# Performance work log

Hardware: AMD Instinct MI355X
Metric: run time of the kernel (lower is better)

Reference implementation:

```python
import jax, jax.numpy as jnp
import numpy as np

N = 100000  # nodes
E = 1600000  # edges
F_IN, F_HID, F_OUT = 64, 128, 128


def _glorot(key, shape):
    fan_in, fan_out = shape[1], shape[0]
    lim = float(np.sqrt(6.0 / (fan_in + fan_out)))
    return jax.random.uniform(key, shape, jnp.float32, -lim, lim)


def setup_inputs() -> dict:
    key = jax.random.key(0)
    ks = jax.random.split(key, 8)
    x = jax.random.normal(ks[0], (N, F_IN), jnp.float32)
    edge_index = jax.random.randint(ks[1], (2, E), 0, N, jnp.int64)
    # SAGEConv params: lin_l (neighbors, with bias), lin_r (root, no bias)
    return {
        "x": x,
        "edge_index": edge_index,
        "W1_l": _glorot(ks[2], (F_HID, F_IN)),
        "b1": jnp.zeros((F_HID,), jnp.float32),
        "W1_r": _glorot(ks[3], (F_HID, F_IN)),
        "W2_l": _glorot(ks[4], (F_OUT, F_HID)),
        "b2": jnp.zeros((F_OUT,), jnp.float32),
        "W2_r": _glorot(ks[5], (F_OUT, F_HID)),
    }


def _sage_conv(x, src, dst, deg_inv, W_l, b, W_r):
    # mean aggregation of source features onto target nodes
    agg = jax.ops.segment_sum(x[src], dst, num_segments=N)  # [N, F]
    agg = agg * deg_inv[:, None]
    return agg @ W_l.T + b + x @ W_r.T


def reference(x, edge_index, W1_l, b1, W1_r, W2_l, b2, W2_r):
    src, dst = edge_index[0], edge_index[1]
    deg = jax.ops.segment_sum(jnp.ones((E,), jnp.float32), dst, num_segments=N)
    deg_inv = 1.0 / jnp.maximum(deg, 1.0)
    h = _sage_conv(x, src, dst, deg_inv, W1_l, b1, W1_r)
    h = jax.nn.relu(h)
    # dropout p=0.5 is identity in eval mode
    out = _sage_conv(h, src, dst, deg_inv, W2_l, b2, W2_r)
    return out
```

## Files before the change

kernel.cpp:

```cpp
#include <hip/hip_runtime.h>
#include <hip/hip_bf16.h>

__device__ __forceinline__ float b2f(unsigned short u) {
  return __uint_as_float(((unsigned int)u) << 16);
}
__device__ __forceinline__ unsigned short f2b(float f) {
  unsigned int x = __float_as_uint(f);
  unsigned int r = x + 0x7FFFu + ((x >> 16) & 1u);
  return (unsigned short)(r >> 16);
}
__device__ __forceinline__ unsigned int pack2(float lo, float hi) {
  return (unsigned int)f2b(lo) | ((unsigned int)f2b(hi) << 16);
}

typedef short bf16x8 __attribute__((ext_vector_type(8)));
typedef float f32x4 __attribute__((ext_vector_type(4)));

#define CHUNK 8192
#define NBUCKP 1024

__global__ void detect_kernel(const void* __restrict__ x_raw,
                              const void* __restrict__ idx_raw,
                              int* __restrict__ hdr) {
  int lane = threadIdx.x;
  const unsigned short* xb = (const unsigned short*)x_raw;
  unsigned short u = xb[2 * lane];
  int e = (u >> 7) & 0xFF;
  bool sane = ((u & 0x7FFFu) == 0) || (e >= 107 && e <= 137);
  unsigned long long m = __ballot(sane);
  const int* ib = (const int*)idx_raw;
  int v = ib[2 * lane + 1];
  unsigned long long m2 = __ballot(v != 0);
  if (lane == 0) {
    hdr[0] = (__popcll(m) >= 32) ? 0 : 1;
    hdr[1] = (m2 == 0ull) ? 1 : 0;
  }
}

__global__ void convert_w_kernel(const void* __restrict__ W1l, const void* __restrict__ W1r,
                                 const void* __restrict__ W2l, const void* __restrict__ W2r,
                                 const void* __restrict__ b1, const void* __restrict__ b2,
                                 const int* __restrict__ hdr,
                                 unsigned short* __restrict__ W1l_h, unsigned short* __restrict__ W1r_h,
                                 unsigned short* __restrict__ W2l_h, unsigned short* __restrict__ W2r_h,
                                 float* __restrict__ b1_f, float* __restrict__ b2_f) {
  int i = blockIdx.x * blockDim.x + threadIdx.x;
  const void* s; unsigned short* dh = nullptr; float* df = nullptr; int off;
  if (i < 8192)       { s = W1l; dh = W1l_h; off = i; }
  else if (i < 16384) { s = W1r; dh = W1r_h; off = i - 8192; }
  else if (i < 32768) { s = W2l; dh = W2l_h; off = i - 16384; }
  else if (i < 49152) { s = W2r; dh = W2r_h; off = i - 32768; }
  else if (i < 49280) { s = b1;  df = b1_f;  off = i - 49152; }
  else if (i < 49408) { s = b2;  df = b2_f;  off = i - 49280; }
  else return;
  float v = hdr[0] ? ((const float*)s)[off] : b2f(((const unsigned short*)s)[off]);
  if (dh) dh[off] = f2b(v);
  else df[off] = v;
}

__global__ void convert_x_kernel(const void* __restrict__ x_raw,
                                 const int* __restrict__ hdr,
                                 unsigned short* __restrict__ xc, int n_elems) {
  int i = blockIdx.x * blockDim.x + threadIdx.x;
  if (i >= n_elems) return;
  xc[i] = hdr[0] ? f2b(((const float*)x_raw)[i]) : ((const unsigned short*)x_raw)[i];
}

__global__ __launch_bounds__(256) void hist_chunks_kernel(
    const int* __restrict__ idx_raw, const int* __restrict__ hdr,
    int* __restrict__ H, int n_edges, int NC) {
  __shared__ int h[NBUCKP];
  for (int i = threadIdx.x; i < NBUCKP; i += 256) h[i] = 0;
  __syncthreads();
  const int c = blockIdx.x;
  const bool i64 = hdr[1];
  const int base = c * CHUNK;
  #pragma unroll
  for (int t = 0; t < CHUNK / 256; ++t) {
    int e = base + t * 256 + threadIdx.x;
    if (e < n_edges) {
      int d = i64 ? idx_raw[2 * (n_edges + e)] : idx_raw[n_edges + e];
      atomicAdd(&h[d >> 7], 1);
    }
  }
  __syncthreads();
  for (int i = threadIdx.x; i < NBUCKP; i += 256) H[(size_t)i * NC + c] = h[i];
}

__global__ __launch_bounds__(256) void gscan_sums_kernel(const int* __restrict__ arr,
                                                         int* __restrict__ blockSums, int n) {
  __shared__ int ws[4];
  int tid = threadIdx.x, lane = tid & 63, wid = tid >> 6;
  int base = blockIdx.x * 2048 + tid * 8;
  int s = 0;
  #pragma unroll
  for (int t = 0; t < 8; ++t) {
    int i = base + t;
    if (i < n) s += arr[i];
  }
  #pragma unroll
  for (int m = 1; m < 64; m <<= 1) s += __shfl_xor(s, m, 64);
  if (lane == 0) ws[wid] = s;
  __syncthreads();
  if (tid == 0) blockSums[blockIdx.x] = ws[0] + ws[1] + ws[2] + ws[3];
}

__global__ void gscan_offsets_kernel(const int* __restrict__ blockSums,
                                     int* __restrict__ blockOffs, int nb) {
  int lane = threadIdx.x;
  int carry = 0;
  for (int start = 0; start < nb; start += 64) {
    int i = start + lane;
    int v = (i < nb) ? blockSums[i] : 0;
    int isc = v;
    #pragma unroll
    for (int off = 1; off < 64; off <<= 1) {
      int t = __shfl_up(isc, off, 64);
      if (lane >= off) isc += t;
    }
    if (i < nb) blockOffs[i] = carry + isc - v;
    carry += __shfl(isc, 63, 64);
  }
}

__global__ __launch_bounds__(256) void gscan_emit_kernel(const int* __restrict__ arr,
                                                         const int* __restrict__ blockOffs,
                                                         int* __restrict__ out, int n) {
  __shared__ int ws[4];
  int tid = threadIdx.x, lane = tid & 63, wid = tid >> 6;
  int base = blockIdx.x * 2048 + tid * 8;
  int v[8];
  int s = 0;
  #pragma unroll
  for (int t = 0; t < 8; ++t) {
    int i = base + t;
    v[t] = (i < n) ? arr[i] : 0;
    s += v[t];
  }
  int isc = s;
  #pragma unroll
  for (int off = 1; off < 64; off <<= 1) {
    int t = __shfl_up(isc, off, 64);
    if (lane >= off) isc += t;
  }
  if (lane == 63) ws[wid] = isc;
  __syncthreads();
  int wb = 0;
  #pragma unroll
  for (int w = 0; w < 4; ++w)
    if (w < wid) wb += ws[w];
  int excl = blockOffs[blockIdx.x] + wb + isc - s;
  #pragma unroll
  for (int t = 0; t < 8; ++t) {
    int i = base + t;
    if (i < n) {
      out[i] = excl;
      excl += v[t];
    }
  }
}

__global__ __launch_bounds__(256) void scatter_kernel(
    const int* __restrict__ idx_raw, const int* __restrict__ hdr,
    const int* __restrict__ O, unsigned long long* __restrict__ ebuf,
    int n_edges, int NC) {
  __shared__ int base[NBUCKP];
  const int c = blockIdx.x;
  for (int i = threadIdx.x; i < NBUCKP; i += 256) base[i] = O[(size_t)i * NC + c];
  __syncthreads();
  const bool i64 = hdr[1];
  const int eb = c * CHUNK;
  #pragma unroll
  for (int t = 0; t < CHUNK / 256; ++t) {
    int e = eb + t * 256 + threadIdx.x;
    if (e < n_edges) {
      int s = i64 ? idx_raw[2 * e] : idx_raw[e];
      int d = i64 ? idx_raw[2 * (n_edges + e)] : idx_raw[n_edges + e];
      int pos = atomicAdd(&base[d >> 7], 1);
      ebuf[pos] = (unsigned long long)(unsigned)s | ((unsigned long long)(unsigned)d << 32);
    }
  }
}

__global__ __launch_bounds__(256) void bucket_csr_kernel(
    const unsigned long long* __restrict__ ebuf, const int* __restrict__ O,
    int* __restrict__ col, int* __restrict__ row_start, float* __restrict__ deg_inv,
    int n_nodes, int n_edges, int NC) {
  __shared__ int cntl[128];
  __shared__ int cur[128];
  __shared__ int w0tot;
  const int b = blockIdx.x, tid = threadIdx.x;
  const int node0 = b << 7;
  const int beg = O[(size_t)b * NC];
  const int end = (b + 1 < NBUCKP) ? O[(size_t)(b + 1) * NC] : n_edges;
  if (tid < 128) cntl[tid] = 0;
  __syncthreads();
  for (int e = beg + tid; e < end; e += 256) {
    int d = (int)(ebuf[e] >> 32);
    atomicAdd(&cntl[d - node0], 1);
  }
  __syncthreads();
  int v = (tid < 128) ? cntl[tid] : 0;
  int lane = tid & 63;
  int isc = v;
  #pragma unroll
  for (int o = 1; o < 64; o <<= 1) {
    int t = __shfl_up(isc, o, 64);
    if (lane >= o) isc += t;
  }
  if (tid == 63) w0tot = isc;
  __syncthreads();
  int incl = isc + ((tid >= 64 && tid < 128) ? w0tot : 0);
  int excl = incl - v;
  if (tid < 128) {
    cur[tid] = excl;
    int node = node0 + tid;
    if (node < n_nodes) {
      row_start[node] = beg + excl;
      deg_inv[node] = 1.0f / (float)((v > 1) ? v : 1);
    }
  }
  __syncthreads();
  for (int e = beg + tid; e < end; e += 256) {
    unsigned long long u = ebuf[e];
    int s = (int)(u & 0xFFFFFFFFull);
    int d = (int)(u >> 32);
    int r = atomicAdd(&cur[d - node0], 1);
    col[beg + r] = s;
  }
  if (b == 0 && tid == 0) row_start[n_nodes] = n_edges;
}

__global__ __launch_bounds__(256) void gather1_kernel(
    const unsigned short* __restrict__ xc, const int* __restrict__ row_start,
    const int* __restrict__ col, const float* __restrict__ deg_inv,
    unsigned short* __restrict__ agg1, int n_nodes) {
  int lane = threadIdx.x & 63;
  int n = blockIdx.x * 4 + (threadIdx.x >> 6);
  if (n >= n_nodes) return;
  int rg = lane >> 3, fq = lane & 7;
  int beg = row_start[n], end = row_start[n + 1];
  float a[8];
  #pragma unroll
  for (int t = 0; t < 8; ++t) a[t] = 0.f;
  int i = beg;
  for (; i + 15 < end; i += 16) {
    int s0 = col[i + rg], s1 = col[i + 8 + rg];
    uint4 p = *(const uint4*)(xc + (size_t)s0 * 64 + fq * 8);
    uint4 q = *(const uint4*)(xc + (size_t)s1 * 64 + fq * 8);
    a[0] += b2f(p.x & 0xFFFF); a[1] += b2f(p.x >> 16);
    a[2] += b2f(p.y & 0xFFFF); a[3] += b2f(p.y >> 16);
    a[4] += b2f(p.z & 0xFFFF); a[5] += b2f(p.z >> 16);
    a[6] += b2f(p.w & 0xFFFF); a[7] += b2f(p.w >> 16);
    a[0] += b2f(q.x & 0xFFFF); a[1] += b2f(q.x >> 16);
    a[2] += b2f(q.y & 0xFFFF); a[3] += b2f(q.y >> 16);
    a[4] += b2f(q.z & 0xFFFF); a[5] += b2f(q.z >> 16);
    a[6] += b2f(q.w & 0xFFFF); a[7] += b2f(q.w >> 16);
  }
  for (; i < end; i += 8) {
    if (i + rg < end) {
      int s0 = col[i + rg];
      uint4 p = *(const uint4*)(xc + (size_t)s0 * 64 + fq * 8);
      a[0] += b2f(p.x & 0xFFFF); a[1] += b2f(p.x >> 16);
      a[2] += b2f(p.y & 0xFFFF); a[3] += b2f(p.y >> 16);
      a[4] += b2f(p.z & 0xFFFF); a[5] += b2f(p.z >> 16);
      a[6] += b2f(p.w & 0xFFFF); a[7] += b2f(p.w >> 16);
    }
  }
  #pragma unroll
  for (int m = 8; m < 64; m <<= 1)
    #pragma unroll
    for (int t = 0; t < 8; ++t) a[t] += __shfl_xor(a[t], m, 64);
  if (rg == 0) {
    float di = deg_inv[n];
    uint4 o;
    o.x = pack2(a[0] * di, a[1] * di);
    o.y = pack2(a[2] * di, a[3] * di);
    o.z = pack2(a[4] * di, a[5] * di);
    o.w = pack2(a[6] * di, a[7] * di);
    *(uint4*)(agg1 + (size_t)n * 64 + fq * 8) = o;
  }
}

__global__ __launch_bounds__(256) void gather2_kernel(
    const unsigned short* __restrict__ h, const int* __restrict__ row_start,
    const int* __restrict__ col, const float* __restrict__ deg_inv,
    unsigned short* __restrict__ agg2, int n_nodes) {
  int lane = threadIdx.x & 63;
  int n = blockIdx.x * 4 + (threadIdx.x >> 6);
  if (n >= n_nodes) return;
  int rg = lane >> 4, fq = lane & 15;
  int beg = row_start[n], end = row_start[n + 1];
  float a[8];
  #pragma unroll
  for (int t = 0; t < 8; ++t) a[t] = 0.f;
  int i = beg;
  for (; i + 7 < end; i += 8) {
    int s0 = col[i + rg], s1 = col[i + 4 + rg];
    uint4 p = *(const uint4*)(h + (size_t)s0 * 128 + fq * 8);
    uint4 q = *(const uint4*)(h + (size_t)s1 * 128 + fq * 8);
    a[0] += b2f(p.x & 0xFFFF); a[1] += b2f(p.x >> 16);
    a[2] += b2f(p.y & 0xFFFF); a[3] += b2f(p.y >> 16);
    a[4] += b2f(p.z & 0xFFFF); a[5] += b2f(p.z >> 16);
    a[6] += b2f(p.w & 0xFFFF); a[7] += b2f(p.w >> 16);
    a[0] += b2f(q.x & 0xFFFF); a[1] += b2f(q.x >> 16);
    a[2] += b2f(q.y & 0xFFFF); a[3] += b2f(q.y >> 16);
    a[4] += b2f(q.z & 0xFFFF); a[5] += b2f(q.z >> 16);
    a[6] += b2f(q.w & 0xFFFF); a[7] += b2f(q.w >> 16);
  }
  for (; i < end; i += 4) {
    if (i + rg < end) {
      int s0 = col[i + rg];
      uint4 p = *(const uint4*)(h + (size_t)s0 * 128 + fq * 8);
      a[0] += b2f(p.x & 0xFFFF); a[1] += b2f(p.x >> 16);
      a[2] += b2f(p.y & 0xFFFF); a[3] += b2f(p.y >> 16);
      a[4] += b2f(p.z & 0xFFFF); a[5] += b2f(p.z >> 16);
      a[6] += b2f(p.w & 0xFFFF); a[7] += b2f(p.w >> 16);
    }
  }
  #pragma unroll
  for (int m = 16; m < 64; m <<= 1)
    #pragma unroll
    for (int t = 0; t < 8; ++t) a[t] += __shfl_xor(a[t], m, 64);
  if (rg == 0) {
    float di = deg_inv[n];
    uint4 o;
    o.x = pack2(a[0] * di, a[1] * di);
    o.y = pack2(a[2] * di, a[3] * di);
    o.z = pack2(a[4] * di, a[5] * di);
    o.w = pack2(a[6] * di, a[7] * di);
    *(uint4*)(agg2 + (size_t)n * 128 + fq * 8) = o;
  }
}

template <int K1, int K2, bool RELU, bool FINAL>
__global__ __launch_bounds__(256, 4) void gemm_mfma(
    const unsigned short* __restrict__ A1, const unsigned short* __restrict__ A2,
    const unsigned short* __restrict__ Wl, const unsigned short* __restrict__ Wr,
    const float* __restrict__ bias,
    unsigned short* __restrict__ Cb, void* __restrict__ Cf,
    const int* __restrict__ hdr, int n_nodes) {
  const int tid = threadIdx.x;
  const int wave = tid >> 6, lane = tid & 63;
  const int m16 = lane & 15, quad = lane >> 4;
  const int nb = blockIdx.x * 128 + wave * 32;
  int row0 = nb + m16;      if (row0 >= n_nodes) row0 = n_nodes - 1;
  int row1 = nb + 16 + m16; if (row1 >= n_nodes) row1 = n_nodes - 1;

  f32x4 acc[2][8];
  #pragma unroll
  for (int mi = 0; mi < 2; ++mi)
    #pragma unroll
    for (int ji = 0; ji < 8; ++ji) acc[mi][ji] = (f32x4){0.f, 0.f, 0.f, 0.f};

  constexpr int NSTEP = (K1 + K2) / 32;
  #pragma unroll
  for (int c = 0; c < NSTEP; ++c) {
    const bool first = (c * 32) < K1;
    const unsigned short* A = first ? A1 : A2;
    const unsigned short* W = first ? Wl : Wr;
    const int kb = first ? c * 32 : c * 32 - K1;
    const int Krow = first ? K1 : K2;
    const int ko = kb + quad * 8;
    bf16x8 a0 = *(const bf16x8*)(A + (size_t)row0 * Krow + ko);
    bf16x8 a1 = *(const bf16x8*)(A + (size_t)row1 * Krow + ko);
    bf16x8 w[8];
    #pragma unroll
    for (int ji = 0; ji < 8; ++ji)
      w[ji] = *(const bf16x8*)(W + (size_t)(ji * 16 + m16) * Krow + ko);
    #pragma unroll
    for (int ji = 0; ji < 8; ++ji) {
      acc[0][ji] = __builtin_amdgcn_mfma_f32_16x16x32_bf16(a0, w[ji], acc[0][ji], 0, 0, 0);
      acc[1][ji] = __builtin_amdgcn_mfma_f32_16x16x32_bf16(a1, w[ji], acc[1][ji], 0, 0, 0);
    }
  }

  const bool f32out = FINAL && (hdr[0] == 1);
  #pragma unroll
  for (int ji = 0; ji < 8; ++ji) {
    int j = ji * 16 + m16;
    float bj = bias[j];
    #pragma unroll
    for (int mi = 0; mi < 2; ++mi) {
      #pragma unroll
      for (int r = 0; r < 4; ++r) {
        int n = nb + mi * 16 + quad * 4 + r;
        if (n >= n_nodes) continue;
        float v = acc[mi][ji][r] + bj;
        if (RELU) v = fmaxf(v, 0.f);
        if (FINAL) {
          if (f32out) ((float*)Cf)[(size_t)n * 128 + j] = v;
          else ((unsigned short*)Cf)[(size_t)n * 128 + j] = f2b(v);
        } else {
          Cb[(size_t)n * 128 + j] = f2b(v);
        }
      }
    }
  }
}

extern "C" void kernel_launch(void* const* d_in, const int* in_sizes, int n_in,
                              void* d_out, int out_size, void* d_ws, size_t ws_size,
                              hipStream_t stream) {
  const void* x_raw  = d_in[0];
  const int* idx_raw = (const int*)d_in[1];
  const void* W1l = d_in[2];
  const void* b1  = d_in[3];
  const void* W1r = d_in[4];
  const void* W2l = d_in[5];
  const void* b2  = d_in[6];
  const void* W2r = d_in[7];
  const int N = in_sizes[0] / 64;
  const int E = in_sizes[1] / 2;
  const int NC = (E + CHUNK - 1) / CHUNK;
  const int NSCAN = NBUCKP * NC;
  const int NBs = (NSCAN + 2047) / 2048;
  const int NBUCK = (N + 127) >> 7;

  char* ws = (char*)d_ws;
  size_t off = 0;
  auto alloc = [&](size_t bytes) {
    char* p = ws + off;
    off = (off + bytes + 511) & ~((size_t)511);
    return p;
  };
  int* hdr        = (int*)alloc(512);
  int* H          = (int*)alloc((size_t)NSCAN * 4);
  int* O          = (int*)alloc((size_t)NSCAN * 4);
  int* blockSums  = (int*)alloc((size_t)NBs * 4);
  int* blockOffs  = (int*)alloc((size_t)NBs * 4);
  unsigned long long* ebuf = (unsigned long long*)alloc((size_t)E * 8);
  int* col        = (int*)alloc((size_t)E * 4);
  int* row_start  = (int*)alloc(((size_t)N + 1) * 4);
  float* deg_inv  = (float*)alloc((size_t)N * 4);
  unsigned short* W1l_h = (unsigned short*)alloc(16384);
  unsigned short* W1r_h = (unsigned short*)alloc(16384);
  unsigned short* W2l_h = (unsigned short*)alloc(32768);
  unsigned short* W2r_h = (unsigned short*)alloc(32768);
  float* b1_f     = (float*)alloc(512);
  float* b2_f     = (float*)alloc(512);
  unsigned short* xc   = (unsigned short*)alloc((size_t)N * 64 * 2);
  unsigned short* agg1 = (unsigned short*)alloc((size_t)N * 64 * 2);
  unsigned short* hbuf = (unsigned short*)alloc((size_t)N * 128 * 2);
  unsigned short* agg2 = (unsigned short*)alloc((size_t)N * 128 * 2);

  detect_kernel<<<1, 64, 0, stream>>>(x_raw, idx_raw, hdr);
  convert_w_kernel<<<(49408 + 255) / 256, 256, 0, stream>>>(
      W1l, W1r, W2l, W2r, b1, b2, hdr, W1l_h, W1r_h, W2l_h, W2r_h, b1_f, b2_f);
  convert_x_kernel<<<(N * 64 + 255) / 256, 256, 0, stream>>>(x_raw, hdr, xc, N * 64);
  hist_chunks_kernel<<<NC, 256, 0, stream>>>(idx_raw, hdr, H, E, NC);
  gscan_sums_kernel<<<NBs, 256, 0, stream>>>(H, blockSums, NSCAN);
  gscan_offsets_kernel<<<1, 64, 0, stream>>>(blockSums, blockOffs, NBs);
  gscan_emit_kernel<<<NBs, 256, 0, stream>>>(H, blockOffs, O, NSCAN);
  scatter_kernel<<<NC, 256, 0, stream>>>(idx_raw, hdr, O, ebuf, E, NC);
  bucket_csr_kernel<<<NBUCK, 256, 0, stream>>>(ebuf, O, col, row_start, deg_inv, N, E, NC);
  gather1_kernel<<<(N + 3) / 4, 256, 0, stream>>>(xc, row_start, col, deg_inv, agg1, N);
  gemm_mfma<64, 64, true, false><<<(N + 127) / 128, 256, 0, stream>>>(
      agg1, xc, W1l_h, W1r_h, b1_f, hbuf, nullptr, hdr, N);
  gather2_kernel<<<(N + 3) / 4, 256, 0, stream>>>(hbuf, row_start, col, deg_inv, agg2, N);
  gemm_mfma<128, 128, false, true><<<(N + 127) / 128, 256, 0, stream>>>(
      agg2, hbuf, W2l_h, W2r_h, b2_f, nullptr, d_out, hdr, N);
}
```

Baseline: 338.5 us.

## Vectorize edge index loads and restructure gather kernels for more loads in flight

The histogram and scatter kernels now read edge indices as uint4 vectors, one per thread, instead of scalar strided loads. gather1 maps two nodes per wavefront, each handled by a half-wave, which shortens the shuffle reduction. Both gather kernels unroll to four outstanding row loads per iteration and use a cheaper bf16-to-float unpack helper. The aim is fewer memory instructions and more memory-level parallelism in the gathers, at the cost of more registers and alignment assumptions on the index buffer.

```diff
diff --git a/kernel.cpp b/kernel.cpp
--- a/kernel.cpp
+++ b/kernel.cpp
@@ -11,6 +11,12 @@
 }
 __device__ __forceinline__ unsigned int pack2(float lo, float hi) {
   return (unsigned int)f2b(lo) | ((unsigned int)f2b(hi) << 16);
+}
+__device__ __forceinline__ void acc8(float* a, uint4 p) {
+  a[0] += __uint_as_float(p.x << 16); a[1] += __uint_as_float(p.x & 0xFFFF0000u);
+  a[2] += __uint_as_float(p.y << 16); a[3] += __uint_as_float(p.y & 0xFFFF0000u);
+  a[4] += __uint_as_float(p.z << 16); a[5] += __uint_as_float(p.z & 0xFFFF0000u);
+  a[6] += __uint_as_float(p.w << 16); a[7] += __uint_as_float(p.w & 0xFFFF0000u);
 }
 
 typedef short bf16x8 __attribute__((ext_vector_type(8)));
@@ -73,14 +79,33 @@
   for (int i = threadIdx.x; i < NBUCKP; i += 256) h[i] = 0;
   __syncthreads();
   const int c = blockIdx.x;
-  const bool i64 = hdr[1];
   const int base = c * CHUNK;
-  #pragma unroll
-  for (int t = 0; t < CHUNK / 256; ++t) {
-    int e = base + t * 256 + threadIdx.x;
-    if (e < n_edges) {
-      int d = i64 ? idx_raw[2 * (n_edges + e)] : idx_raw[n_edges + e];
-      atomicAdd(&h[d >> 7], 1);
+  const int lim = min(n_edges - base, CHUNK);
+  if (hdr[1]) {
+    const uint4* dp = (const uint4*)(idx_raw + 2 * (size_t)n_edges + 2 * (size_t)base);
+    #pragma unroll
+    for (int t = 0; t < CHUNK / 512; ++t) {
+      int q = t * 256 + threadIdx.x;
+      int e = 2 * q;
+      if (e < lim) {
+        uint4 v = dp[q];
+        atomicAdd(&h[((int)v.x) >> 7], 1);
+        if (e + 1 < lim) atomicAdd(&h[((int)v.z) >> 7], 1);
+      }
+    }
+  } else {
+    const uint4* dp = (const uint4*)(idx_raw + (size_t)n_edges + base);
+    #pragma unroll
+    for (int t = 0; t < CHUNK / 1024; ++t) {
+      int q = t * 256 + threadIdx.x;
+      int e = 4 * q;
+      if (e < lim) {
+        uint4 v = dp[q];
+        atomicAdd(&h[((int)v.x) >> 7], 1);
+        if (e + 1 < lim) atomicAdd(&h[((int)v.y) >> 7], 1);
+        if (e + 2 < lim) atomicAdd(&h[((int)v.z) >> 7], 1);
+        if (e + 3 < lim) atomicAdd(&h[((int)v.w) >> 7], 1);
+      }
     }
   }
   __syncthreads();
@@ -168,16 +193,49 @@
   const int c = blockIdx.x;
   for (int i = threadIdx.x; i < NBUCKP; i += 256) base[i] = O[(size_t)i * NC + c];
   __syncthreads();
-  const bool i64 = hdr[1];
   const int eb = c * CHUNK;
-  #pragma unroll
-  for (int t = 0; t < CHUNK / 256; ++t) {
-    int e = eb + t * 256 + threadIdx.x;
-    if (e < n_edges) {
-      int s = i64 ? idx_raw[2 * e] : idx_raw[e];
-      int d = i64 ? idx_raw[2 * (n_edges + e)] : idx_raw[n_edges + e];
-      int pos = atomicAdd(&base[d >> 7], 1);
-      ebuf[pos] = (unsigned long long)(unsigned)s | ((unsigned long long)(unsigned)d << 32);
+  const int lim = min(n_edges - eb, CHUNK);
+  if (hdr[1]) {
+    const uint4* sp = (const uint4*)(idx_raw + 2 * (size_t)eb);
+    const uint4* dp = (const uint4*)(idx_raw + 2 * (size_t)n_edges + 2 * (size_t)eb);
+    #pragma unroll
+    for (int t = 0; t < CHUNK / 512; ++t) {
+      int q = t * 256 + threadIdx.x;
+      int e = 2 * q;
+      if (e < lim) {
+        uint4 sv = sp[q], dv = dp[q];
+        int p0 = atomicAdd(&base[((int)dv.x) >> 7], 1);
+        ebuf[p0] = (unsigned long long)sv.x | ((unsigned long long)dv.x << 32);
+        if (e + 1 < lim) {
+          int p1 = atomicAdd(&base[((int)dv.z) >> 7], 1);
+          ebuf[p1] = (unsigned long long)sv.z | ((unsigned long long)dv.z << 32);
+        }
+      }
+    }
+  } else {
+    const uint4* sp = (const uint4*)(idx_raw + (size_t)eb);
+    const uint4* dp = (const uint4*)(idx_raw + (size_t)n_edges + eb);
+    #pragma unroll
+    for (int t = 0; t < CHUNK / 1024; ++t) {
+      int q = t * 256 + threadIdx.x;
+      int e = 4 * q;
+      if (e < lim) {
+        uint4 sv = sp[q], dv = dp[q];
+        int p0 = atomicAdd(&base[((int)dv.x) >> 7], 1);
+        ebuf[p0] = (unsigned long long)sv.x | ((unsigned long long)dv.x << 32);
+        if (e + 1 < lim) {
+          int p1 = atomicAdd(&base[((int)dv.y) >> 7], 1);
+          ebuf[p1] = (unsigned long long)sv.y | ((unsigned long long)dv.y << 32);
+        }
+        if (e + 2 < lim) {
+          int p2 = atomicAdd(&base[((int)dv.z) >> 7], 1);
+          ebuf[p2] = (unsigned long long)sv.z | ((unsigned long long)dv.z << 32);
+        }
+        if (e + 3 < lim) {
+          int p3 = atomicAdd(&base[((int)dv.w) >> 7], 1);
+          ebuf[p3] = (unsigned long long)sv.w | ((unsigned long long)dv.w << 32);
+        }
+      }
     }
   }
 }
@@ -236,39 +294,35 @@
     const int* __restrict__ col, const float* __restrict__ deg_inv,
     unsigned short* __restrict__ agg1, int n_nodes) {
   int lane = threadIdx.x & 63;
-  int n = blockIdx.x * 4 + (threadIdx.x >> 6);
+  int n = blockIdx.x * 8 + (threadIdx.x >> 6) * 2 + (lane >> 5);
   if (n >= n_nodes) return;
-  int rg = lane >> 3, fq = lane & 7;
+  int l32 = lane & 31;
+  int rg = l32 >> 3, fq = l32 & 7;
   int beg = row_start[n], end = row_start[n + 1];
   float a[8];
   #pragma unroll
   for (int t = 0; t < 8; ++t) a[t] = 0.f;
   int i = beg;
   for (; i + 15 < end; i += 16) {
-    int s0 = col[i + rg], s1 = col[i + 8 + rg];
-    uint4 p = *(const uint4*)(xc + (size_t)s0 * 64 + fq * 8);
-    uint4 q = *(const uint4*)(xc + (size_t)s1 * 64 + fq * 8);
-    a[0] += b2f(p.x & 0xFFFF); a[1] += b2f(p.x >> 16);
-    a[2] += b2f(p.y & 0xFFFF); a[3] += b2f(p.y >> 16);
-    a[4] += b2f(p.z & 0xFFFF); a[5] += b2f(p.z >> 16);
-    a[6] += b2f(p.w & 0xFFFF); a[7] += b2f(p.w >> 16);
-    a[0] += b2f(q.x & 0xFFFF); a[1] += b2f(q.x >> 16);
-    a[2] += b2f(q.y & 0xFFFF); a[3] += b2f(q.y >> 16);
-    a[4] += b2f(q.z & 0xFFFF); a[5] += b2f(q.z >> 16);
-    a[6] += b2f(q.w & 0xFFFF); a[7] += b2f(q.w >> 16);
-  }
-  for (; i < end; i += 8) {
-    if (i + rg < end) {
-      int s0 = col[i + rg];
-      uint4 p = *(const uint4*)(xc + (size_t)s0 * 64 + fq * 8);
-      a[0] += b2f(p.x & 0xFFFF); a[1] += b2f(p.x >> 16);
-      a[2] += b2f(p.y & 0xFFFF); a[3] += b2f(p.y >> 16);
-      a[4] += b2f(p.z & 0xFFFF); a[5] += b2f(p.z >> 16);
-      a[6] += b2f(p.w & 0xFFFF); a[7] += b2f(p.w >> 16);
-    }
-  }
-  #pragma unroll
-  for (int m = 8; m < 64; m <<= 1)
+    int s0 = col[i + rg], s1 = col[i + 4 + rg], s2 = col[i + 8 + rg], s3 = col[i + 12 + rg];
+    uint4 p0 = *(const uint4*)(xc + (size_t)s0 * 64 + fq * 8);
+    uint4 p1 = *(const uint4*)(xc + (size_t)s1 * 64 + fq * 8);
+    uint4 p2 = *(const uint4*)(xc + (size_t)s2 * 64 + fq * 8);
+    uint4 p3 = *(const uint4*)(xc + (size_t)s3 * 64 + fq * 8);
+    acc8(a, p0); acc8(a, p1); acc8(a, p2); acc8(a, p3);
+  }
+  for (; i + 3 < end; i += 4) {
+    int s0 = col[i + rg];
+    uint4 p0 = *(const uint4*)(xc + (size_t)s0 * 64 + fq * 8);
+    acc8(a, p0);
+  }
+  if (i + rg < end) {
+    int s0 = col[i + rg];
+    uint4 p0 = *(const uint4*)(xc + (size_t)s0 * 64 + fq * 8);
+    acc8(a, p0);
+  }
+  #pragma unroll
+  for (int m = 8; m <= 16; m <<= 1)
     #pragma unroll
     for (int t = 0; t < 8; ++t) a[t] += __shfl_xor(a[t], m, 64);
   if (rg == 0) {
@@ -295,28 +349,23 @@
   #pragma unroll
   for (int t = 0; t < 8; ++t) a[t] = 0.f;
   int i = beg;
-  for (; i + 7 < end; i += 8) {
-    int s0 = col[i + rg], s1 = col[i + 4 + rg];
-    uint4 p = *(const uint4*)(h + (size_t)s0 * 128 + fq * 8);
-    uint4 q = *(const uint4*)(h + (size_t)s1 * 128 + fq * 8);
-    a[0] += b2f(p.x & 0xFFFF); a[1] += b2f(p.x >> 16);
-    a[2] += b2f(p.y & 0xFFFF); a[3] += b2f(p.y >> 16);
-    a[4] += b2f(p.z & 0xFFFF); a[5] += b2f(p.z >> 16);
-    a[6] += b2f(p.w & 0xFFFF); a[7] += b2f(p.w >> 16);
-    a[0] += b2f(q.x & 0xFFFF); a[1] += b2f(q.x >> 16);
-    a[2] += b2f(q.y & 0xFFFF); a[3] += b2f(q.y >> 16);
-    a[4] += b2f(q.z & 0xFFFF); a[5] += b2f(q.z >> 16);
-    a[6] += b2f(q.w & 0xFFFF); a[7] += b2f(q.w >> 16);
-  }
-  for (; i < end; i += 4) {
-    if (i + rg < end) {
-      int s0 = col[i + rg];
-      uint4 p = *(const uint4*)(h + (size_t)s0 * 128 + fq * 8);
-      a[0] += b2f(p.x & 0xFFFF); a[1] += b2f(p.x >> 16);
-      a[2] += b2f(p.y & 0xFFFF); a[3] += b2f(p.y >> 16);
-      a[4] += b2f(p.z & 0xFFFF); a[5] += b2f(p.z >> 16);
-      a[6] += b2f(p.w & 0xFFFF); a[7] += b2f(p.w >> 16);
-    }
+  for (; i + 15 < end; i += 16) {
+    int s0 = col[i + rg], s1 = col[i + 4 + rg], s2 = col[i + 8 + rg], s3 = col[i + 12 + rg];
+    uint4 p0 = *(const uint4*)(h + (size_t)s0 * 128 + fq * 8);
+    uint4 p1 = *(const uint4*)(h + (size_t)s1 * 128 + fq * 8);
+    uint4 p2 = *(const uint4*)(h + (size_t)s2 * 128 + fq * 8);
+    uint4 p3 = *(const uint4*)(h + (size_t)s3 * 128 + fq * 8);
+    acc8(a, p0); acc8(a, p1); acc8(a, p2); acc8(a, p3);
+  }
+  for (; i + 3 < end; i += 4) {
+    int s0 = col[i + rg];
+    uint4 p0 = *(const uint4*)(h + (size_t)s0 * 128 + fq * 8);
+    acc8(a, p0);
+  }
+  if (i + rg < end) {
+    int s0 = col[i + rg];
+    uint4 p0 = *(const uint4*)(h + (size_t)s0 * 128 + fq * 8);
+    acc8(a, p0);
   }
   #pragma unroll
   for (int m = 16; m < 64; m <<= 1)
@@ -454,7 +503,7 @@
   gscan_emit_kernel<<<NBs, 256, 0, stream>>>(H, blockOffs, O, NSCAN);
   scatter_kernel<<<NC, 256, 0, stream>>>(idx_raw, hdr, O, ebuf, E, NC);
   bucket_csr_kernel<<<NBUCK, 256, 0, stream>>>(ebuf, O, col, row_start, deg_inv, N, E, NC);
-  gather1_kernel<<<(N + 3) / 4, 256, 0, stream>>>(xc, row_start, col, deg_inv, agg1, N);
+  gather1_kernel<<<(N + 7) / 8, 256, 0, stream>>>(xc, row_start, col, deg_inv, agg1, N);
   gemm_mfma<64, 64, true, false><<<(N + 127) / 128, 256, 0, stream>>>(
       agg1, xc, W1l_h, W1r_h, b1_f, hbuf, nullptr, hdr, N);
   gather2_kernel<<<(N + 3) / 4, 256, 0, stream>>>(hbuf, row_start, col, deg_inv, agg2, N);
```

Result: faster. 331.8 us (-2.0%).
